# Optimization experiments

Hardware: AMD Instinct MI355X
Metric: run time of the kernel (lower is better)

The kernel has to match this reference:

```python
import jax, jax.numpy as jnp
import numpy as np

B, D, N, S = 4096, 768, 8192, 4  # batch, embedding_dim, len(y)==cat rows, source_size


def setup_inputs() -> dict:
    key = jax.random.key(0)
    k1, k2, k3, k4 = jax.random.split(key, 4)
    batch_x = jax.random.normal(k1, (B, D), dtype=jnp.float32)
    cat = jax.random.normal(k2, (N, D), dtype=jnp.float32)
    y = jax.random.randint(k3, (N,), 0, 2, dtype=jnp.int32)
    # phi_srcs: xavier-uniform-like scale for (D, 1) params, stacked as [S, D]
    phi = jax.random.normal(k4, (S, D), dtype=jnp.float32) * 0.05
    bias = jnp.zeros((1,), dtype=jnp.float32)
    return {"batch_x": batch_x, "cat": cat, "y": y, "phi": phi, "bias": bias}


def reference(batch_x, cat, y, phi, bias):
    # con[n, b] = cat[n] . batch_x[b]   -> [N, B]
    con = jnp.einsum('nd,bd->nb', cat, batch_x)
    # F.normalize(con, p=4, dim=0): divide each column by its 4-norm (eps=1e-12)
    norm4 = jnp.power(jnp.sum(jnp.abs(con) ** 4, axis=0), 0.25)
    con = con / jnp.maximum(norm4, 1e-12)
    # softmax over all N rows (dim=0), per batch column
    con = jax.nn.softmax(con, axis=0)
    # chunk into S sources along the N axis: psi [S, N/S, B]
    psi = con.reshape(S, N // S, B)
    yf = y.astype(jnp.float32).reshape(S, N // S)  # y chunks [S, N/S]
    # theta_s = exp(x @ phi_s): [S, B]  (unnormalized, as in the original output path)
    theta = jnp.exp(jnp.einsum('bd,sd->sb', batch_x, phi))
    # per-source: sum_n y[s,n] * psi[s,n,b], then scale by theta[s,b]; sum over sources
    sum_matrix = jnp.sum(jnp.einsum('sn,snb->sb', yf, psi) * theta, axis=0)  # [B]
    y_hat = jax.nn.sigmoid(sum_matrix + bias)  # bias [1] broadcasts -> [B]
    return y_hat
```

## Files before the change

kernel.cpp:

```cpp
#include <hip/hip_runtime.h>
#include <hip/hip_bf16.h>
#include <stdint.h>

#define Bdim 4096
#define Ddim 768
#define Ndim 8192
#define Sdim 4

typedef __attribute__((ext_vector_type(4))) float floatx4;
typedef __attribute__((ext_vector_type(8))) int int8v;
typedef __attribute__((ext_vector_type(4))) int int4v;

__device__ inline unsigned short f2bf(float f) {
  unsigned u = __builtin_bit_cast(unsigned, f);
  unsigned r = (u + 0x7fffu + ((u >> 16) & 1u)) >> 16;
  return (unsigned short)r;
}
__device__ inline float bf2f(unsigned short s) {
  return __builtin_bit_cast(float, (unsigned)s << 16);
}

__device__ inline int pack_fp8x4(float4 v) {
  int r = __builtin_amdgcn_cvt_pk_fp8_f32(v.x, v.y, 0, 0);
  r = __builtin_amdgcn_cvt_pk_fp8_f32(v.z, v.w, r, 1);
  return r;
}

__device__ inline void async_copy16(const void* g, void* l) {
  __builtin_amdgcn_global_load_lds(
      (__attribute__((address_space(1))) void*)(g),
      (__attribute__((address_space(3))) void*)(l),
      16, 0, 0);
}

__global__ void convert_kernel(const float* __restrict__ x,
                               const float* __restrict__ cat,
                               const float* __restrict__ phi,
                               unsigned char* __restrict__ xq,
                               unsigned char* __restrict__ catq,
                               float* __restrict__ stats,
                               float* __restrict__ theta) {
  int gid = blockIdx.x * blockDim.x + threadIdx.x;
  int stride = gridDim.x * blockDim.x;
  const int nx4 = (Bdim * Ddim) / 4;
  const int nc4 = (Ndim * Ddim) / 4;
  for (int i = gid; i < nx4; i += stride)
    ((int*)xq)[i] = pack_fp8x4(((const float4*)x)[i]);
  for (int i = gid; i < nc4; i += stride)
    ((int*)catq)[i] = pack_fp8x4(((const float4*)cat)[i]);
  if (gid < 6 * Bdim) stats[gid] = 0.0f;

  int gw = gid >> 6;
  int lane = threadIdx.x & 63;
  if (gw < Bdim) {
    const float* xr = x + (size_t)gw * Ddim;
    float a0 = 0.f, a1 = 0.f, a2 = 0.f, a3 = 0.f;
    for (int d = lane; d < Ddim; d += 64) {
      float xv = xr[d];
      a0 = fmaf(xv, phi[d], a0);
      a1 = fmaf(xv, phi[Ddim + d], a1);
      a2 = fmaf(xv, phi[2 * Ddim + d], a2);
      a3 = fmaf(xv, phi[3 * Ddim + d], a3);
    }
#pragma unroll
    for (int off = 32; off > 0; off >>= 1) {
      a0 += __shfl_down(a0, off);
      a1 += __shfl_down(a1, off);
      a2 += __shfl_down(a2, off);
      a3 += __shfl_down(a3, off);
    }
    if (lane == 0) {
      theta[gw] = __expf(a0);
      theta[Bdim + gw] = __expf(a1);
      theta[2 * Bdim + gw] = __expf(a2);
      theta[3 * Bdim + gw] = __expf(a3);
    }
  }
}

__global__ __launch_bounds__(256) void gemm_bt_kernel(
    const unsigned char* __restrict__ A,
    const unsigned char* __restrict__ Bm,
    unsigned short* __restrict__ C,
    float* __restrict__ s4) {
  __shared__ unsigned char As[128 * 128];
  __shared__ unsigned char Bs[128 * 128];

  const int tid = threadIdx.x;
  const int wave = tid >> 6;
  const int lane = tid & 63;
  const int quad = lane >> 4;
  const int l16 = lane & 15;
  const int wm = (wave & 1) * 64;
  const int wn = (wave >> 1) * 64;
  const int m0 = blockIdx.x * 128;
  const int n0 = blockIdx.y * 128;

  floatx4 acc[4][4];
#pragma unroll
  for (int i = 0; i < 4; ++i)
#pragma unroll
    for (int j = 0; j < 4; ++j) acc[i][j] = (floatx4){0.f, 0.f, 0.f, 0.f};

  const unsigned char* a_src[4];
  const unsigned char* b_src[4];
#pragma unroll
  for (int i = 0; i < 4; ++i) {
    int p = tid + 256 * i;
    int row = ((p >> 6) << 3) + (p & 7);
    int colb = ((p >> 3) & 7) * 16;
    a_src[i] = A + (size_t)(m0 + row) * Ddim + colb;
    b_src[i] = Bm + (size_t)(n0 + row) * Ddim + colb;
  }

  for (int k0 = 0; k0 < Ddim; k0 += 128) {
#pragma unroll
    for (int i = 0; i < 4; ++i) {
      async_copy16(a_src[i] + k0, As + (tid + 256 * i) * 16);
      async_copy16(b_src[i] + k0, Bs + (tid + 256 * i) * 16);
    }
    __syncthreads();

    int8v af[4], bf[4];
#pragma unroll
    for (int mi = 0; mi < 4; ++mi) {
      int r = wm + mi * 16 + l16;
      int base = ((r >> 3) << 10) + quad * 256 + (r & 7) * 16;
      int4v lo = *(const int4v*)(As + base);
      int4v hi = *(const int4v*)(As + base + 128);
      af[mi] = __builtin_shufflevector(lo, hi, 0, 1, 2, 3, 4, 5, 6, 7);
    }
#pragma unroll
    for (int ni = 0; ni < 4; ++ni) {
      int r = wn + ni * 16 + l16;
      int base = ((r >> 3) << 10) + quad * 256 + (r & 7) * 16;
      int4v lo = *(const int4v*)(Bs + base);
      int4v hi = *(const int4v*)(Bs + base + 128);
      bf[ni] = __builtin_shufflevector(lo, hi, 0, 1, 2, 3, 4, 5, 6, 7);
    }
#pragma unroll
    for (int mi = 0; mi < 4; ++mi)
#pragma unroll
      for (int ni = 0; ni < 4; ++ni)
        acc[mi][ni] = __builtin_amdgcn_mfma_scale_f32_16x16x128_f8f6f4(
            af[mi], bf[ni], acc[mi][ni], 0, 0,
            0, 0x7f7f7f7f,
            0, 0x7f7f7f7f);
    __syncthreads();
  }

  float cs4[4] = {0.f, 0.f, 0.f, 0.f};
#pragma unroll
  for (int mi = 0; mi < 4; ++mi)
#pragma unroll
    for (int ni = 0; ni < 4; ++ni) {
      int row = m0 + wm + mi * 16 + quad * 4;
      int col = n0 + wn + ni * 16 + l16;
#pragma unroll
      for (int rr = 0; rr < 4; ++rr) {
        float cv = acc[mi][ni][rr];
        C[(size_t)(row + rr) * Bdim + col] = f2bf(cv);
        float c2 = cv * cv;
        cs4[ni] += c2 * c2;
      }
    }
#pragma unroll
  for (int ni = 0; ni < 4; ++ni) {
    float v = cs4[ni];
    v += __shfl_xor(v, 16);
    v += __shfl_xor(v, 32);
    if (quad == 0) atomicAdd(&s4[n0 + wn + ni * 16 + l16], v);
  }
}

__global__ void expsum_kernel(const unsigned short* __restrict__ con,
                              const float* __restrict__ s4,
                              const int* __restrict__ y,
                              float* __restrict__ denom,
                              float* __restrict__ numer) {
  int col0 = blockIdx.x * 1024 + threadIdx.x * 4;
  int n0 = blockIdx.y * 64;
  int src = n0 / (Ndim / Sdim);

  float4 s = *(const float4*)(s4 + col0);
  float inv0 = 1.0f / fmaxf(sqrtf(sqrtf(s.x)), 1e-12f);
  float inv1 = 1.0f / fmaxf(sqrtf(sqrtf(s.y)), 1e-12f);
  float inv2 = 1.0f / fmaxf(sqrtf(sqrtf(s.z)), 1e-12f);
  float inv3 = 1.0f / fmaxf(sqrtf(sqrtf(s.w)), 1e-12f);

  const unsigned short* p = con + (size_t)n0 * Bdim + col0;
  float d0 = 0.f, d1 = 0.f, d2 = 0.f, d3 = 0.f;
  float m0 = 0.f, m1 = 0.f, m2 = 0.f, m3 = 0.f;
#pragma unroll 8
  for (int i = 0; i < 64; ++i) {
    ushort4 v = *(const ushort4*)(p + (size_t)i * Bdim);
    float yv = (float)y[n0 + i];
    float e0 = __expf(bf2f(v.x) * inv0);
    float e1 = __expf(bf2f(v.y) * inv1);
    float e2 = __expf(bf2f(v.z) * inv2);
    float e3 = __expf(bf2f(v.w) * inv3);
    d0 += e0; d1 += e1; d2 += e2; d3 += e3;
    m0 += e0 * yv; m1 += e1 * yv; m2 += e2 * yv; m3 += e3 * yv;
  }
  atomicAdd(&denom[col0 + 0], d0);
  atomicAdd(&denom[col0 + 1], d1);
  atomicAdd(&denom[col0 + 2], d2);
  atomicAdd(&denom[col0 + 3], d3);
  float* np = numer + (size_t)src * Bdim + col0;
  atomicAdd(np + 0, m0);
  atomicAdd(np + 1, m1);
  atomicAdd(np + 2, m2);
  atomicAdd(np + 3, m3);
}

__global__ void finalize_kernel(const float* __restrict__ denom,
                                const float* __restrict__ numer,
                                const float* __restrict__ theta,
                                const float* __restrict__ bias,
                                float* __restrict__ out) {
  int b = blockIdx.x * 256 + threadIdx.x;
  float acc = 0.f;
#pragma unroll
  for (int si = 0; si < Sdim; ++si)
    acc += numer[si * Bdim + b] * theta[si * Bdim + b];
  float z = acc / denom[b] + bias[0];
  out[b] = 1.0f / (1.0f + __expf(-z));
}

extern "C" void kernel_launch(void* const* d_in, const int* in_sizes, int n_in,
                              void* d_out, int out_size, void* d_ws,
                              size_t ws_size, hipStream_t stream) {
  const float* batch_x = (const float*)d_in[0];
  const float* cat = (const float*)d_in[1];
  const int* y = (const int*)d_in[2];
  const float* phi = (const float*)d_in[3];
  const float* bias = (const float*)d_in[4];
  float* out = (float*)d_out;

  char* ws = (char*)d_ws;
  unsigned char* catq = (unsigned char*)ws;
  unsigned char* xq = catq + (size_t)Ndim * Ddim;
  unsigned short* con = (unsigned short*)(xq + (size_t)Bdim * Ddim);
  float* stats = (float*)(con + (size_t)Ndim * Bdim);
  float* s4 = stats;
  float* denom = s4 + Bdim;
  float* numer = denom + Bdim;
  float* theta = stats + 6 * Bdim;

  convert_kernel<<<2048, 256, 0, stream>>>(batch_x, cat, phi, xq, catq, stats,
                                           theta);

  dim3 g2(Ndim / 128, Bdim / 128);
  gemm_bt_kernel<<<g2, 256, 0, stream>>>(catq, xq, con, s4);

  dim3 g3(Bdim / 1024, Ndim / 64);
  expsum_kernel<<<g3, 256, 0, stream>>>(con, s4, y, denom, numer);

  finalize_kernel<<<Bdim / 256, 256, 0, stream>>>(denom, numer, theta, bias,
                                                  out);
}
```

Measured before the change: 177.1 us.

## Double-buffer LDS tiles in fp8 GEMM to overlap global loads with MFMA

Splits the GEMM's shared-memory tiles into two buffers and issues async global-to-LDS copies for the next K-slice before computing the current one. Partial vmcnt waits (8 outstanding) replace full syncs, so load latency is meant to hide behind MFMA work. LDS use doubles to 64KB per block, which may cut occupancy. The hand-encoded waitcnt values and raw barriers also carry a correctness risk if the encoding does not match the architecture.

Result: slower. 180.7 us (+2.1%).

```diff
diff --git a/kernel.cpp b/kernel.cpp
--- a/kernel.cpp
+++ b/kernel.cpp
@@ -10,6 +10,9 @@
 typedef __attribute__((ext_vector_type(4))) float floatx4;
 typedef __attribute__((ext_vector_type(8))) int int8v;
 typedef __attribute__((ext_vector_type(4))) int int4v;
+
+#define WAIT_VM8 0x0F78
+#define WAIT_VM0 0x0F70
 
 __device__ inline unsigned short f2bf(float f) {
   unsigned u = __builtin_bit_cast(unsigned, f);
@@ -83,8 +86,8 @@
     const unsigned char* __restrict__ Bm,
     unsigned short* __restrict__ C,
     float* __restrict__ s4) {
-  __shared__ unsigned char As[128 * 128];
-  __shared__ unsigned char Bs[128 * 128];
+  __shared__ unsigned char As[2][128 * 128];
+  __shared__ unsigned char Bs[2][128 * 128];
 
   const int tid = threadIdx.x;
   const int wave = tid >> 6;
@@ -113,29 +116,43 @@
     b_src[i] = Bm + (size_t)(n0 + row) * Ddim + colb;
   }
 
-  for (int k0 = 0; k0 < Ddim; k0 += 128) {
-#pragma unroll
-    for (int i = 0; i < 4; ++i) {
-      async_copy16(a_src[i] + k0, As + (tid + 256 * i) * 16);
-      async_copy16(b_src[i] + k0, Bs + (tid + 256 * i) * 16);
-    }
-    __syncthreads();
+#pragma unroll
+  for (int i = 0; i < 4; ++i) {
+    async_copy16(a_src[i], As[0] + (tid + 256 * i) * 16);
+    async_copy16(b_src[i], Bs[0] + (tid + 256 * i) * 16);
+  }
+
+#pragma unroll
+  for (int kk = 0; kk < 6; ++kk) {
+    const int p = kk & 1;
+    if (kk < 5) {
+      const int k0 = (kk + 1) * 128;
+#pragma unroll
+      for (int i = 0; i < 4; ++i) {
+        async_copy16(a_src[i] + k0, As[1 - p] + (tid + 256 * i) * 16);
+        async_copy16(b_src[i] + k0, Bs[1 - p] + (tid + 256 * i) * 16);
+      }
+      __builtin_amdgcn_s_waitcnt(WAIT_VM8);
+    } else {
+      __builtin_amdgcn_s_waitcnt(WAIT_VM0);
+    }
+    __builtin_amdgcn_s_barrier();
 
     int8v af[4], bf[4];
 #pragma unroll
     for (int mi = 0; mi < 4; ++mi) {
       int r = wm + mi * 16 + l16;
       int base = ((r >> 3) << 10) + quad * 256 + (r & 7) * 16;
-      int4v lo = *(const int4v*)(As + base);
-      int4v hi = *(const int4v*)(As + base + 128);
+      int4v lo = *(const int4v*)(As[p] + base);
+      int4v hi = *(const int4v*)(As[p] + base + 128);
       af[mi] = __builtin_shufflevector(lo, hi, 0, 1, 2, 3, 4, 5, 6, 7);
     }
 #pragma unroll
     for (int ni = 0; ni < 4; ++ni) {
       int r = wn + ni * 16 + l16;
       int base = ((r >> 3) << 10) + quad * 256 + (r & 7) * 16;
-      int4v lo = *(const int4v*)(Bs + base);
-      int4v hi = *(const int4v*)(Bs + base + 128);
+      int4v lo = *(const int4v*)(Bs[p] + base);
+      int4v hi = *(const int4v*)(Bs[p] + base + 128);
       bf[ni] = __builtin_shufflevector(lo, hi, 0, 1, 2, 3, 4, 5, 6, 7);
     }
 #pragma unroll
@@ -146,7 +163,8 @@
             af[mi], bf[ni], acc[mi][ni], 0, 0,
             0, 0x7f7f7f7f,
             0, 0x7f7f7f7f);
-    __syncthreads();
+
+    __builtin_amdgcn_s_barrier();
   }
 
   float cs4[4] = {0.f, 0.f, 0.f, 0.f};
```

## Store GEMM output as packed fp8 in row-grouped layout for expsum

Applied to the files above, without the earlier changes.

The intermediate con matrix is now stored as fp8 instead of bf16. Each 32-bit word packs four consecutive rows for one column, which halves the intermediate write and read traffic. The expsum kernel is restructured to match: one column per thread, it reads the packed words, loads y as int4, and uses fewer, larger row groups per block. This lowers the precision of the stored logits before exp, which risks accuracy loss in the softmax numerator and denominator.

Measured after the change: 157.1 us. 1.13x faster.

```diff
diff --git a/kernel.cpp b/kernel.cpp
--- a/kernel.cpp
+++ b/kernel.cpp
@@ -10,15 +10,6 @@
 typedef __attribute__((ext_vector_type(4))) float floatx4;
 typedef __attribute__((ext_vector_type(8))) int int8v;
 typedef __attribute__((ext_vector_type(4))) int int4v;
-
-__device__ inline unsigned short f2bf(float f) {
-  unsigned u = __builtin_bit_cast(unsigned, f);
-  unsigned r = (u + 0x7fffu + ((u >> 16) & 1u)) >> 16;
-  return (unsigned short)r;
-}
-__device__ inline float bf2f(unsigned short s) {
-  return __builtin_bit_cast(float, (unsigned)s << 16);
-}
 
 __device__ inline int pack_fp8x4(float4 v) {
   int r = __builtin_amdgcn_cvt_pk_fp8_f32(v.x, v.y, 0, 0);
@@ -81,7 +72,7 @@
 __global__ __launch_bounds__(256) void gemm_bt_kernel(
     const unsigned char* __restrict__ A,
     const unsigned char* __restrict__ Bm,
-    unsigned short* __restrict__ C,
+    unsigned int* __restrict__ Cw,
     float* __restrict__ s4) {
   __shared__ unsigned char As[128 * 128];
   __shared__ unsigned char Bs[128 * 128];
@@ -154,13 +145,15 @@
   for (int mi = 0; mi < 4; ++mi)
 #pragma unroll
     for (int ni = 0; ni < 4; ++ni) {
-      int row = m0 + wm + mi * 16 + quad * 4;
+      int g = (m0 + wm + mi * 16) / 4 + quad;
       int col = n0 + wn + ni * 16 + l16;
+      floatx4 a = acc[mi][ni];
+      int w = __builtin_amdgcn_cvt_pk_fp8_f32(a[0], a[1], 0, 0);
+      w = __builtin_amdgcn_cvt_pk_fp8_f32(a[2], a[3], w, 1);
+      Cw[(size_t)g * Bdim + col] = (unsigned int)w;
 #pragma unroll
       for (int rr = 0; rr < 4; ++rr) {
-        float cv = acc[mi][ni][rr];
-        C[(size_t)(row + rr) * Bdim + col] = f2bf(cv);
-        float c2 = cv * cv;
+        float c2 = a[rr] * a[rr];
         cs4[ni] += c2 * c2;
       }
     }
@@ -173,44 +166,32 @@
   }
 }
 
-__global__ void expsum_kernel(const unsigned short* __restrict__ con,
+__global__ void expsum_kernel(const unsigned int* __restrict__ conq,
                               const float* __restrict__ s4,
                               const int* __restrict__ y,
                               float* __restrict__ denom,
                               float* __restrict__ numer) {
-  int col0 = blockIdx.x * 1024 + threadIdx.x * 4;
-  int n0 = blockIdx.y * 64;
-  int src = n0 / (Ndim / Sdim);
-
-  float4 s = *(const float4*)(s4 + col0);
-  float inv0 = 1.0f / fmaxf(sqrtf(sqrtf(s.x)), 1e-12f);
-  float inv1 = 1.0f / fmaxf(sqrtf(sqrtf(s.y)), 1e-12f);
-  float inv2 = 1.0f / fmaxf(sqrtf(sqrtf(s.z)), 1e-12f);
-  float inv3 = 1.0f / fmaxf(sqrtf(sqrtf(s.w)), 1e-12f);
-
-  const unsigned short* p = con + (size_t)n0 * Bdim + col0;
-  float d0 = 0.f, d1 = 0.f, d2 = 0.f, d3 = 0.f;
-  float m0 = 0.f, m1 = 0.f, m2 = 0.f, m3 = 0.f;
-#pragma unroll 8
+  int b = blockIdx.x * 256 + threadIdx.x;
+  int g0 = blockIdx.y * 64;
+  int src = (g0 * 4) / (Ndim / Sdim);
+
+  float inv = 1.0f / fmaxf(sqrtf(sqrtf(s4[b])), 1e-12f);
+  const unsigned int* p = conq + (size_t)g0 * Bdim + b;
+  float dsum = 0.f, nsum = 0.f;
+#pragma unroll 4
   for (int i = 0; i < 64; ++i) {
-    ushort4 v = *(const ushort4*)(p + (size_t)i * Bdim);
-    float yv = (float)y[n0 + i];
-    float e0 = __expf(bf2f(v.x) * inv0);
-    float e1 = __expf(bf2f(v.y) * inv1);
-    float e2 = __expf(bf2f(v.z) * inv2);
-    float e3 = __expf(bf2f(v.w) * inv3);
-    d0 += e0; d1 += e1; d2 += e2; d3 += e3;
-    m0 += e0 * yv; m1 += e1 * yv; m2 += e2 * yv; m3 += e3 * yv;
-  }
-  atomicAdd(&denom[col0 + 0], d0);
-  atomicAdd(&denom[col0 + 1], d1);
-  atomicAdd(&denom[col0 + 2], d2);
-  atomicAdd(&denom[col0 + 3], d3);
-  float* np = numer + (size_t)src * Bdim + col0;
-  atomicAdd(np + 0, m0);
-  atomicAdd(np + 1, m1);
-  atomicAdd(np + 2, m2);
-  atomicAdd(np + 3, m3);
+    unsigned int w = p[(size_t)i * Bdim];
+    int4 yv = *(const int4*)(y + 4 * (g0 + i));
+    float e0 = __expf(__builtin_amdgcn_cvt_f32_fp8(w, 0) * inv);
+    float e1 = __expf(__builtin_amdgcn_cvt_f32_fp8(w, 1) * inv);
+    float e2 = __expf(__builtin_amdgcn_cvt_f32_fp8(w, 2) * inv);
+    float e3 = __expf(__builtin_amdgcn_cvt_f32_fp8(w, 3) * inv);
+    dsum += e0 + e1 + e2 + e3;
+    nsum += e0 * (float)yv.x + e1 * (float)yv.y + e2 * (float)yv.z +
+            e3 * (float)yv.w;
+  }
+  atomicAdd(&denom[b], dsum);
+  atomicAdd(&numer[src * Bdim + b], nsum);
 }
 
 __global__ void finalize_kernel(const float* __restrict__ denom,
@@ -240,8 +221,8 @@
   char* ws = (char*)d_ws;
   unsigned char* catq = (unsigned char*)ws;
   unsigned char* xq = catq + (size_t)Ndim * Ddim;
-  unsigned short* con = (unsigned short*)(xq + (size_t)Bdim * Ddim);
-  float* stats = (float*)(con + (size_t)Ndim * Bdim);
+  unsigned int* conq = (unsigned int*)(xq + (size_t)Bdim * Ddim);
+  float* stats = (float*)((unsigned char*)conq + (size_t)Ndim * Bdim);
   float* s4 = stats;
   float* denom = s4 + Bdim;
   float* numer = denom + Bdim;
@@ -251,10 +232,10 @@
                                            theta);
 
   dim3 g2(Ndim / 128, Bdim / 128);
-  gemm_bt_kernel<<<g2, 256, 0, stream>>>(catq, xq, con, s4);
-
-  dim3 g3(Bdim / 1024, Ndim / 64);
-  expsum_kernel<<<g3, 256, 0, stream>>>(con, s4, y, denom, numer);
+  gemm_bt_kernel<<<g2, 256, 0, stream>>>(catq, xq, conq, s4);
+
+  dim3 g3(Bdim / 256, 32);
+  expsum_kernel<<<g3, 256, 0, stream>>>(conq, s4, y, denom, numer);
 
   finalize_kernel<<<Bdim / 256, 256, 0, stream>>>(denom, numer, theta, bias,
                                                   out);
```
